# Kernel optimization log

Hardware: AMD Instinct MI355X
Metric: run time of the kernel (lower is better)

## Reference

```python
import itertools
import jax, jax.numpy as jnp
import numpy as np

VOLSHAPE = (160, 192, 160)  # D, H, W (SynthSeg-style 3D crop)
NDIMS = 3
BATCH = 4
CHANNELS = 1


def setup_inputs() -> dict:
    key = jax.random.key(0)
    k1, k2 = jax.random.split(key)
    vol = jax.random.normal(k1, (BATCH, *VOLSHAPE, CHANNELS), dtype=jnp.float32)
    # affine near identity: layer treats trf as (roughly) the full 4x4 matrix applied
    # to centered coordinates; affine_to_shift subtracts the centered mesh.
    trf = jnp.eye(NDIMS + 1, dtype=jnp.float32)[None] \
        + 0.05 * jax.random.normal(k2, (BATCH, NDIMS + 1, NDIMS + 1), dtype=jnp.float32)
    return {"vol": vol, "trf": trf}


def _meshgrid(volshape):
    ranges = [jnp.arange(s, dtype=jnp.float32) for s in volshape]
    return jnp.stack(jnp.meshgrid(*ranges, indexing='ij'), axis=-1)  # [D,H,W,3]


def _affine_to_shift(A, volshape):
    # A: [4,4]; faithful to neuron.utils.affine_to_shift with shift_center=True
    mesh = _meshgrid(volshape)                                        # [D,H,W,3]
    center = jnp.array([(s - 1) / 2.0 for s in volshape], dtype=jnp.float32)
    mesh_c = mesh - center                                            # centered mesh
    flat = mesh_c.reshape(-1, NDIMS)                                  # [V,3]
    flat1 = jnp.concatenate([flat, jnp.ones((flat.shape[0], 1), flat.dtype)], axis=1)  # [V,4]
    loc = flat1 @ A[:NDIMS].T                                         # [V,3] = (A[:3] @ mesh^T)^T
    return loc.reshape(*volshape, NDIMS) - mesh_c                     # shift field


def _interpn_linear(vol, loc):
    # vol: [D,H,W,C]; loc: [D,H,W,3] absolute sample locations
    volshape = vol.shape[:-1]
    C = vol.shape[-1]
    max_loc = jnp.array([d - 1 for d in volshape], dtype=jnp.float32)
    loc0 = jnp.floor(loc)
    clipped = jnp.clip(loc, 0.0, max_loc)
    loc0c = jnp.clip(loc0, 0.0, max_loc)
    loc1c = jnp.clip(loc0c + 1.0, 0.0, max_loc)
    d1 = loc1c - clipped           # weight for corner bit 0 (neuron's reversed ordering)
    d0 = 1.0 - d1                  # weight for corner bit 1
    i0 = loc0c.astype(jnp.int32)
    i1 = loc1c.astype(jnp.int32)
    strides = np.array([volshape[1] * volshape[2], volshape[2], 1], dtype=np.int32)
    vol_flat = vol.reshape(-1, C)
    out = jnp.zeros((*volshape, C), dtype=vol.dtype)
    for corner in itertools.product((0, 1), repeat=NDIMS):
        idx = jnp.zeros(volshape, dtype=jnp.int32)
        wt = jnp.ones(volshape, dtype=vol.dtype)
        for d in range(NDIMS):
            ii = (i0 if corner[d] == 0 else i1)[..., d]
            idx = idx + ii * int(strides[d])
            wt = wt * (d1 if corner[d] == 0 else d0)[..., d]
        gathered = vol_flat[idx.reshape(-1)].reshape(*volshape, C)
        out = out + wt[..., None] * gathered
    return out


def reference(vol, trf):
    volshape = vol.shape[1:-1]

    def single(v, A):
        shift = _affine_to_shift(A, volshape)          # affine -> dense shift field
        loc = _meshgrid(volshape) + shift              # transform(): mesh + shift
        return _interpn_linear(v, loc)

    return jax.vmap(single)(vol, trf)
```

## Files before the change

### kernel.cpp

```cpp
#include <hip/hip_runtime.h>

constexpr int D = 160, H = 192, W = 160, B = 4;
constexpr int V  = D * H * W;
constexpr int HW = H * W;

struct DimS { int i0; float w0; };

__device__ __forceinline__ DimS prep(float loc, float maxv, int maxi) {
    float c  = fminf(fmaxf(loc, 0.0f), maxv);
    int  i0  = min((int)c, maxi - 1);
    DimS s;
    s.i0 = i0;
    s.w0 = (float)(i0 + 1) - c;
    return s;
}

__device__ __forceinline__ float trilerp(const float* __restrict__ vb,
                                         DimS sd, DimS sh, DimS sw) {
    const float* p0 = vb + ((sd.i0 * H + sh.i0) * W + sw.i0);
    float2 v00, v01, v10, v11;
    __builtin_memcpy(&v00, p0,          8);
    __builtin_memcpy(&v01, p0 + W,      8);
    __builtin_memcpy(&v10, p0 + HW,     8);
    __builtin_memcpy(&v11, p0 + HW + W, 8);
    const float pd00 = fmaf(sw.w0, v00.x - v00.y, v00.y);
    const float pd01 = fmaf(sw.w0, v01.x - v01.y, v01.y);
    const float pd10 = fmaf(sw.w0, v10.x - v10.y, v10.y);
    const float pd11 = fmaf(sw.w0, v11.x - v11.y, v11.y);
    const float q0 = fmaf(sh.w0, pd00 - pd01, pd01);
    const float q1 = fmaf(sh.w0, pd10 - pd11, pd11);
    return fmaf(sd.w0, q0 - q1, q1);
}

__global__ __launch_bounds__(256) void st_affine_kernel(
        const float* __restrict__ vol, const float* __restrict__ trf,
        float* __restrict__ out) {
    const int b  = blockIdx.z;
    const int d0 = blockIdx.y * 2;
    const int hblk = blockIdx.x / 5;
    const int wblk = blockIdx.x - hblk * 5;
    const int w = wblk * 32 + threadIdx.x;
    const int h = hblk * 8  + threadIdx.y;

    const float* __restrict__ A = trf + b * 16;
    const float a00 = A[0], a01 = A[1], a02 = A[2],  a03 = A[3];
    const float a10 = A[4], a11 = A[5], a12 = A[6],  a13 = A[7];
    const float a20 = A[8], a21 = A[9], a22 = A[10], a23 = A[11];

    constexpr float cd = (D - 1) * 0.5f;
    constexpr float ch = (H - 1) * 0.5f;
    constexpr float cw = (W - 1) * 0.5f;

    const float md = (float)d0 - cd;
    const float mh = (float)h  - ch;
    const float mw = (float)w  - cw;

    const float ld0 = cd + fmaf(a00, md, fmaf(a01, mh, fmaf(a02, mw, a03)));
    const float lh0 = ch + fmaf(a10, md, fmaf(a11, mh, fmaf(a12, mw, a13)));
    const float lw0 = cw + fmaf(a20, md, fmaf(a21, mh, fmaf(a22, mw, a23)));
    const float ld1 = ld0 + a00;
    const float lh1 = lh0 + a10;
    const float lw1 = lw0 + a20;

    const DimS sd0 = prep(ld0, (float)(D - 1), D - 1);
    const DimS sh0 = prep(lh0, (float)(H - 1), H - 1);
    const DimS sw0 = prep(lw0, (float)(W - 1), W - 1);
    const DimS sd1 = prep(ld1, (float)(D - 1), D - 1);
    const DimS sh1 = prep(lh1, (float)(H - 1), H - 1);
    const DimS sw1 = prep(lw1, (float)(W - 1), W - 1);

    const float* __restrict__ vb = vol + (size_t)b * V;

    const float r0 = trilerp(vb, sd0, sh0, sw0);
    const float r1 = trilerp(vb, sd1, sh1, sw1);

    float* ob = out + (size_t)b * V + (size_t)h * W + w;
    __builtin_nontemporal_store(r0, ob + (size_t)d0 * HW);
    __builtin_nontemporal_store(r1, ob + (size_t)(d0 + 1) * HW);
}

extern "C" void kernel_launch(void* const* d_in, const int* in_sizes, int n_in,
                              void* d_out, int out_size, void* d_ws, size_t ws_size,
                              hipStream_t stream) {
    const float* vol = (const float*)d_in[0];
    const float* trf = (const float*)d_in[1];
    float* out = (float*)d_out;

    dim3 grid((H / 8) * (W / 32), D / 2, B);
    dim3 block(32, 8, 1);
    st_affine_kernel<<<grid, block, 0, stream>>>(vol, trf, out);
}
```

Baseline: 171.8 us.

## Process four depth voxels per thread with batched loads and XCD-aware block remap

Each thread now handles four consecutive depth slices instead of two, and issues all gather loads before a scheduling barrier and then does the interpolation math. This raises memory-level parallelism per thread. The grid is flattened to 1D and block IDs are remapped so contiguous tiles land on the same XCD, which is meant to improve L2 locality of the gathered neighborhoods. In exchange it uses more registers per thread and launches half as many blocks.

```diff
diff --git a/kernel.cpp b/kernel.cpp
--- a/kernel.cpp
+++ b/kernel.cpp
@@ -3,6 +3,12 @@
 constexpr int D = 160, H = 192, W = 160, B = 4;
 constexpr int V  = D * H * W;
 constexpr int HW = H * W;
+constexpr int VPT = 4;
+constexpr int GX  = (H / 8) * (W / 32);
+constexpr int GY  = D / VPT;
+constexpr int NWG = GX * GY * B;
+constexpr int NXCD = 8;
+constexpr int CPX  = NWG / NXCD;
 
 struct DimS { int i0; float w0; };
 
@@ -15,34 +21,29 @@
     return s;
 }
 
-__device__ __forceinline__ float trilerp(const float* __restrict__ vb,
-                                         DimS sd, DimS sh, DimS sw) {
-    const float* p0 = vb + ((sd.i0 * H + sh.i0) * W + sw.i0);
-    float2 v00, v01, v10, v11;
-    __builtin_memcpy(&v00, p0,          8);
-    __builtin_memcpy(&v01, p0 + W,      8);
-    __builtin_memcpy(&v10, p0 + HW,     8);
-    __builtin_memcpy(&v11, p0 + HW + W, 8);
-    const float pd00 = fmaf(sw.w0, v00.x - v00.y, v00.y);
-    const float pd01 = fmaf(sw.w0, v01.x - v01.y, v01.y);
-    const float pd10 = fmaf(sw.w0, v10.x - v10.y, v10.y);
-    const float pd11 = fmaf(sw.w0, v11.x - v11.y, v11.y);
-    const float q0 = fmaf(sh.w0, pd00 - pd01, pd01);
-    const float q1 = fmaf(sh.w0, pd10 - pd11, pd11);
-    return fmaf(sd.w0, q0 - q1, q1);
+__device__ __forceinline__ float2 ld2(const float* __restrict__ p) {
+    float2 v;
+    __builtin_memcpy(&v, p, 8);
+    return v;
 }
 
 __global__ __launch_bounds__(256) void st_affine_kernel(
         const float* __restrict__ vol, const float* __restrict__ trf,
         float* __restrict__ out) {
-    const int b  = blockIdx.z;
-    const int d0 = blockIdx.y * 2;
-    const int hblk = blockIdx.x / 5;
-    const int wblk = blockIdx.x - hblk * 5;
+    const int id  = blockIdx.x;
+    const int nid = (id & (NXCD - 1)) * CPX + (id >> 3);
+    const int bz  = nid / (GX * GY);
+    const int rem = nid - bz * (GX * GY);
+    const int by  = rem / GX;
+    const int bx  = rem - by * GX;
+
+    const int d0   = by * VPT;
+    const int hblk = bx / 5;
+    const int wblk = bx - hblk * 5;
     const int w = wblk * 32 + threadIdx.x;
     const int h = hblk * 8  + threadIdx.y;
 
-    const float* __restrict__ A = trf + b * 16;
+    const float* __restrict__ A = trf + bz * 16;
     const float a00 = A[0], a01 = A[1], a02 = A[2],  a03 = A[3];
     const float a10 = A[4], a11 = A[5], a12 = A[6],  a13 = A[7];
     const float a20 = A[8], a21 = A[9], a22 = A[10], a23 = A[11];
@@ -55,28 +56,41 @@
     const float mh = (float)h  - ch;
     const float mw = (float)w  - cw;
 
-    const float ld0 = cd + fmaf(a00, md, fmaf(a01, mh, fmaf(a02, mw, a03)));
-    const float lh0 = ch + fmaf(a10, md, fmaf(a11, mh, fmaf(a12, mw, a13)));
-    const float lw0 = cw + fmaf(a20, md, fmaf(a21, mh, fmaf(a22, mw, a23)));
-    const float ld1 = ld0 + a00;
-    const float lh1 = lh0 + a10;
-    const float lw1 = lw0 + a20;
+    float ld = cd + fmaf(a00, md, fmaf(a01, mh, fmaf(a02, mw, a03)));
+    float lh = ch + fmaf(a10, md, fmaf(a11, mh, fmaf(a12, mw, a13)));
+    float lw = cw + fmaf(a20, md, fmaf(a21, mh, fmaf(a22, mw, a23)));
 
-    const DimS sd0 = prep(ld0, (float)(D - 1), D - 1);
-    const DimS sh0 = prep(lh0, (float)(H - 1), H - 1);
-    const DimS sw0 = prep(lw0, (float)(W - 1), W - 1);
-    const DimS sd1 = prep(ld1, (float)(D - 1), D - 1);
-    const DimS sh1 = prep(lh1, (float)(H - 1), H - 1);
-    const DimS sw1 = prep(lw1, (float)(W - 1), W - 1);
+    const float* __restrict__ vb = vol + (size_t)bz * V;
 
-    const float* __restrict__ vb = vol + (size_t)b * V;
+    DimS sd[VPT], sh[VPT], sw[VPT];
+    float2 v00[VPT], v01[VPT], v10[VPT], v11[VPT];
 
-    const float r0 = trilerp(vb, sd0, sh0, sw0);
-    const float r1 = trilerp(vb, sd1, sh1, sw1);
+#pragma unroll
+    for (int k = 0; k < VPT; ++k) {
+        sd[k] = prep(ld, (float)(D - 1), D - 1);
+        sh[k] = prep(lh, (float)(H - 1), H - 1);
+        sw[k] = prep(lw, (float)(W - 1), W - 1);
+        const float* p = vb + ((sd[k].i0 * H + sh[k].i0) * W + sw[k].i0);
+        v00[k] = ld2(p);
+        v01[k] = ld2(p + W);
+        v10[k] = ld2(p + HW);
+        v11[k] = ld2(p + HW + W);
+        ld += a00; lh += a10; lw += a20;
+    }
+    __builtin_amdgcn_sched_barrier(0);
 
-    float* ob = out + (size_t)b * V + (size_t)h * W + w;
-    __builtin_nontemporal_store(r0, ob + (size_t)d0 * HW);
-    __builtin_nontemporal_store(r1, ob + (size_t)(d0 + 1) * HW);
+    float* ob = out + (size_t)bz * V + (size_t)h * W + w;
+#pragma unroll
+    for (int k = 0; k < VPT; ++k) {
+        const float pd00 = fmaf(sw[k].w0, v00[k].x - v00[k].y, v00[k].y);
+        const float pd01 = fmaf(sw[k].w0, v01[k].x - v01[k].y, v01[k].y);
+        const float pd10 = fmaf(sw[k].w0, v10[k].x - v10[k].y, v10[k].y);
+        const float pd11 = fmaf(sw[k].w0, v11[k].x - v11[k].y, v11[k].y);
+        const float q0 = fmaf(sh[k].w0, pd00 - pd01, pd01);
+        const float q1 = fmaf(sh[k].w0, pd10 - pd11, pd11);
+        const float r  = fmaf(sd[k].w0, q0 - q1, q1);
+        __builtin_nontemporal_store(r, ob + (size_t)(d0 + k) * HW);
+    }
 }
 
 extern "C" void kernel_launch(void* const* d_in, const int* in_sizes, int n_in,
@@ -86,7 +100,7 @@
     const float* trf = (const float*)d_in[1];
     float* out = (float*)d_out;
 
-    dim3 grid((H / 8) * (W / 32), D / 2, B);
+    dim3 grid(NWG, 1, 1);
     dim3 block(32, 8, 1);
     st_affine_kernel<<<grid, block, 0, stream>>>(vol, trf, out);
 }
```

After: 180.4 us. 1.05x slower.

## Stage each block's source bounding box into LDS via global_load_lds before trilinear gathers

Applied to the files above, without the earlier changes.

Each block computes the bounding box of source voxels its 32x8x4 output tile can touch under the affine map. When that box fits a fixed LDS capacity, it copies the box into shared memory with direct global-to-LDS loads and gathers the eight corners from LDS. Otherwise it falls back to the original global gathers. It also raises outputs per thread from 2 to 4 along depth and builds sample locations incrementally. The aim is to cut scattered global/L2 gather traffic, at the cost of a bulk copy per block, a barrier, and LDS bank conflicts.

```diff
diff --git a/kernel.cpp b/kernel.cpp
--- a/kernel.cpp
+++ b/kernel.cpp
@@ -3,6 +3,13 @@
 constexpr int D = 160, H = 192, W = 160, B = 4;
 constexpr int V  = D * H * W;
 constexpr int HW = H * W;
+constexpr int VPT = 4;
+constexpr int TW  = 32, TH = 8;
+constexpr int GXW = W / TW;
+constexpr int GXH = H / TH;
+constexpr int SD_CAP = 14, SH_CAP = 14, SW_CAP = 40;
+constexpr int PLANE = SH_CAP * SW_CAP;
+constexpr int LDS_FLOATS = SD_CAP * PLANE;
 
 struct DimS { int i0; float w0; };
 
@@ -15,14 +22,9 @@
     return s;
 }
 
-__device__ __forceinline__ float trilerp(const float* __restrict__ vb,
-                                         DimS sd, DimS sh, DimS sw) {
-    const float* p0 = vb + ((sd.i0 * H + sh.i0) * W + sw.i0);
-    float2 v00, v01, v10, v11;
-    __builtin_memcpy(&v00, p0,          8);
-    __builtin_memcpy(&v01, p0 + W,      8);
-    __builtin_memcpy(&v10, p0 + HW,     8);
-    __builtin_memcpy(&v11, p0 + HW + W, 8);
+__device__ __forceinline__ float lerp3(DimS sd, DimS sh, DimS sw,
+                                       float2 v00, float2 v01,
+                                       float2 v10, float2 v11) {
     const float pd00 = fmaf(sw.w0, v00.x - v00.y, v00.y);
     const float pd01 = fmaf(sw.w0, v01.x - v01.y, v01.y);
     const float pd10 = fmaf(sw.w0, v10.x - v10.y, v10.y);
@@ -32,15 +34,36 @@
     return fmaf(sd.w0, q0 - q1, q1);
 }
 
+__device__ __forceinline__ float trilerp_g(const float* __restrict__ vb,
+                                           DimS sd, DimS sh, DimS sw) {
+    const float* p0 = vb + ((sd.i0 * H + sh.i0) * W + sw.i0);
+    float2 v00, v01, v10, v11;
+    __builtin_memcpy(&v00, p0,          8);
+    __builtin_memcpy(&v01, p0 + W,      8);
+    __builtin_memcpy(&v10, p0 + HW,     8);
+    __builtin_memcpy(&v11, p0 + HW + W, 8);
+    return lerp3(sd, sh, sw, v00, v01, v10, v11);
+}
+
+__device__ __forceinline__ void gload_lds_row(const float* g, float* l) {
+    __builtin_amdgcn_global_load_lds(
+        (const __attribute__((address_space(1))) void*)g,
+        (__attribute__((address_space(3))) void*)l,
+        4, 0, 0);
+}
+
 __global__ __launch_bounds__(256) void st_affine_kernel(
         const float* __restrict__ vol, const float* __restrict__ trf,
         float* __restrict__ out) {
+    __shared__ float sm[LDS_FLOATS];
+
     const int b  = blockIdx.z;
-    const int d0 = blockIdx.y * 2;
-    const int hblk = blockIdx.x / 5;
-    const int wblk = blockIdx.x - hblk * 5;
-    const int w = wblk * 32 + threadIdx.x;
-    const int h = hblk * 8  + threadIdx.y;
+    const int d0 = blockIdx.y * VPT;
+    const int hblk = blockIdx.x / GXW;
+    const int wblk = blockIdx.x - hblk * GXW;
+    const int w0 = wblk * TW, h0 = hblk * TH;
+    const int w  = w0 + threadIdx.x;
+    const int h  = h0 + threadIdx.y;
 
     const float* __restrict__ A = trf + b * 16;
     const float a00 = A[0], a01 = A[1], a02 = A[2],  a03 = A[3];
@@ -51,32 +74,77 @@
     constexpr float ch = (H - 1) * 0.5f;
     constexpr float cw = (W - 1) * 0.5f;
 
-    const float md = (float)d0 - cd;
-    const float mh = (float)h  - ch;
-    const float mw = (float)w  - cw;
+    const float md0 = (float)d0 - cd, mh0 = (float)h0 - ch, mw0 = (float)w0 - cw;
+    const float od = cd + fmaf(a00, md0, fmaf(a01, mh0, fmaf(a02, mw0, a03)));
+    const float oh = ch + fmaf(a10, md0, fmaf(a11, mh0, fmaf(a12, mw0, a13)));
+    const float ow = cw + fmaf(a20, md0, fmaf(a21, mh0, fmaf(a22, mw0, a23)));
 
-    const float ld0 = cd + fmaf(a00, md, fmaf(a01, mh, fmaf(a02, mw, a03)));
-    const float lh0 = ch + fmaf(a10, md, fmaf(a11, mh, fmaf(a12, mw, a13)));
-    const float lw0 = cw + fmaf(a20, md, fmaf(a21, mh, fmaf(a22, mw, a23)));
-    const float ld1 = ld0 + a00;
-    const float lh1 = lh0 + a10;
-    const float lw1 = lw0 + a20;
+    const float Ed = (float)(VPT - 1), Eh = (float)(TH - 1), Ew = (float)(TW - 1);
+    const float dn = od + fminf(a00*Ed,0.f) + fminf(a01*Eh,0.f) + fminf(a02*Ew,0.f);
+    const float dx = od + fmaxf(a00*Ed,0.f) + fmaxf(a01*Eh,0.f) + fmaxf(a02*Ew,0.f);
+    const float hn = oh + fminf(a10*Ed,0.f) + fminf(a11*Eh,0.f) + fminf(a12*Ew,0.f);
+    const float hx = oh + fmaxf(a10*Ed,0.f) + fmaxf(a11*Eh,0.f) + fmaxf(a12*Ew,0.f);
+    const float wn = ow + fminf(a20*Ed,0.f) + fminf(a21*Eh,0.f) + fminf(a22*Ew,0.f);
+    const float wx = ow + fmaxf(a20*Ed,0.f) + fmaxf(a21*Eh,0.f) + fmaxf(a22*Ew,0.f);
 
-    const DimS sd0 = prep(ld0, (float)(D - 1), D - 1);
-    const DimS sh0 = prep(lh0, (float)(H - 1), H - 1);
-    const DimS sw0 = prep(lw0, (float)(W - 1), W - 1);
-    const DimS sd1 = prep(ld1, (float)(D - 1), D - 1);
-    const DimS sh1 = prep(lh1, (float)(H - 1), H - 1);
-    const DimS sw1 = prep(lw1, (float)(W - 1), W - 1);
+    const int lo_d = min((int)fminf(fmaxf(dn, 0.f), (float)(D-1)), D - 2);
+    const int hi_d = min((int)fminf(fmaxf(dx, 0.f), (float)(D-1)), D - 2) + 1;
+    const int lo_h = min((int)fminf(fmaxf(hn, 0.f), (float)(H-1)), H - 2);
+    const int hi_h = min((int)fminf(fmaxf(hx, 0.f), (float)(H-1)), H - 2) + 1;
+    const int lo_w = min((int)fminf(fmaxf(wn, 0.f), (float)(W-1)), W - 2);
+    const int hi_w = min((int)fminf(fmaxf(wx, 0.f), (float)(W-1)), W - 2) + 1;
+    const int SDn = hi_d - lo_d + 1;
+    const int SHn = hi_h - lo_h + 1;
+    const int SWn = hi_w - lo_w + 1;
+
+    const float fy = (float)threadIdx.y, fx = (float)threadIdx.x;
+    float ld = fmaf(a01, fy, fmaf(a02, fx, od));
+    float lh = fmaf(a11, fy, fmaf(a12, fx, oh));
+    float lw = fmaf(a21, fy, fmaf(a22, fx, ow));
 
     const float* __restrict__ vb = vol + (size_t)b * V;
+    float* ob = out + (size_t)b * V + (size_t)h * W + w;
 
-    const float r0 = trilerp(vb, sd0, sh0, sw0);
-    const float r1 = trilerp(vb, sd1, sh1, sw1);
+    if (SDn <= SD_CAP && SHn <= SH_CAP && SWn <= SW_CAP) {
+        const int tid  = threadIdx.y * TW + threadIdx.x;
+        const int wv   = tid >> 6;
+        const int lane = tid & 63;
+        for (int z = 0; z < SDn; ++z) {
+            const float* gz = vb + (size_t)(lo_d + z) * HW + lo_w;
+            for (int y = wv; y < SHn; y += 4) {
+                if (lane < SWn)
+                    gload_lds_row(gz + (size_t)(lo_h + y) * W + lane,
+                                  &sm[(z * SH_CAP + y) * SW_CAP]);
+            }
+        }
+        __syncthreads();
 
-    float* ob = out + (size_t)b * V + (size_t)h * W + w;
-    __builtin_nontemporal_store(r0, ob + (size_t)d0 * HW);
-    __builtin_nontemporal_store(r1, ob + (size_t)(d0 + 1) * HW);
+        const int offL = (lo_d * SH_CAP + lo_h) * SW_CAP + lo_w;
+#pragma unroll
+        for (int k = 0; k < VPT; ++k) {
+            const DimS sd = prep(ld, (float)(D - 1), D - 1);
+            const DimS sh = prep(lh, (float)(H - 1), H - 1);
+            const DimS sw = prep(lw, (float)(W - 1), W - 1);
+            const int idx = (sd.i0 * SH_CAP + sh.i0) * SW_CAP + sw.i0 - offL;
+            const float2 v00 = make_float2(sm[idx],                  sm[idx + 1]);
+            const float2 v01 = make_float2(sm[idx + SW_CAP],         sm[idx + SW_CAP + 1]);
+            const float2 v10 = make_float2(sm[idx + PLANE],          sm[idx + PLANE + 1]);
+            const float2 v11 = make_float2(sm[idx + PLANE + SW_CAP], sm[idx + PLANE + SW_CAP + 1]);
+            const float r = lerp3(sd, sh, sw, v00, v01, v10, v11);
+            __builtin_nontemporal_store(r, ob + (size_t)(d0 + k) * HW);
+            ld += a00; lh += a10; lw += a20;
+        }
+    } else {
+#pragma unroll
+        for (int k = 0; k < VPT; ++k) {
+            const DimS sd = prep(ld, (float)(D - 1), D - 1);
+            const DimS sh = prep(lh, (float)(H - 1), H - 1);
+            const DimS sw = prep(lw, (float)(W - 1), W - 1);
+            const float r = trilerp_g(vb, sd, sh, sw);
+            __builtin_nontemporal_store(r, ob + (size_t)(d0 + k) * HW);
+            ld += a00; lh += a10; lw += a20;
+        }
+    }
 }
 
 extern "C" void kernel_launch(void* const* d_in, const int* in_sizes, int n_in,
@@ -86,7 +154,7 @@
     const float* trf = (const float*)d_in[1];
     float* out = (float*)d_out;
 
-    dim3 grid((H / 8) * (W / 32), D / 2, B);
-    dim3 block(32, 8, 1);
+    dim3 grid(GXH * GXW, D / VPT, B);
+    dim3 block(TW, TH, 1);
     st_affine_kernel<<<grid, block, 0, stream>>>(vol, trf, out);
 }
```

Result: faster. 161.2 us (-6.2%).
